# Kernel optimization log

Measured on AMD Instinct MI355X. Metric: run time of the kernel, lower is better.

## Reference

```python
import jax, jax.numpy as jnp
import numpy as np

LAMBDA_1 = 1.0
LAMBDA_2 = 0.5


def setup_inputs() -> dict:
    key = jax.random.key(0)
    k1, k2, k3, k4, k5 = jax.random.split(key, 5)
    N_TRAIN, N_UNL, C = 4096, 32768, 1000
    G, K = 512, 64
    return {
        "train_logits": jax.random.normal(k1, (N_TRAIN, C), dtype=jnp.float32),
        "train_targets": jax.random.randint(k2, (N_TRAIN,), 0, C, dtype=jnp.int64),
        "unlabeled_logits": jax.random.normal(k3, (N_UNL, C), dtype=jnp.float32),
        "centroid_ids": jax.random.randint(k4, (G,), 0, N_TRAIN, dtype=jnp.int64),
        "member_ids": jax.random.randint(k5, (G, K), 0, N_UNL, dtype=jnp.int64),
    }


def reference(train_logits, train_targets, unlabeled_logits, centroid_ids, member_ids):
    N_unl = unlabeled_logits.shape[0]
    G, K = member_ids.shape

    # --- cross-entropy (mean) ---
    logp = jax.nn.log_softmax(train_logits, axis=-1)
    ce = -jnp.mean(jnp.take_along_axis(logp, train_targets[:, None], axis=1))

    # --- gather group tensors ---
    centroids = train_logits[centroid_ids]          # [G, C]
    members = unlabeled_logits[member_ids]          # [G, K, C]

    # --- alignment: sum_g sum_k ||centroid_g - member_gk||_2 / N_unl ---
    align = jnp.sum(jnp.linalg.norm(centroids[:, None, :] - members, axis=-1)) / N_unl

    # --- robustness: per-group upper-triangle pairwise L2 sums / (K * N_unl) ---
    sq = jnp.sum(members * members, axis=-1)                       # [G, K]
    gram = jnp.einsum("gkc,glc->gkl", members, members)            # [G, K, K]
    d2 = jnp.maximum(sq[:, :, None] + sq[:, None, :] - 2.0 * gram, 0.0)
    dist = jnp.sqrt(jnp.where(d2 > 0, d2, 1.0)) * (d2 > 0)         # safe sqrt
    iu = jnp.triu(jnp.ones((K, K), dtype=dist.dtype), k=1)         # i < j pairs
    robust = jnp.sum(dist * iu) / (K * N_unl)

    return ce + LAMBDA_1 * align + LAMBDA_2 * robust
```

## Files before the change

kernel.cpp:

```cpp
#include <hip/hip_runtime.h>
#include <hip/hip_bf16.h>

#define N_TRAIN 4096
#define N_UNL   32768
#define C_DIM   1000
#define G_GRP   512
#define K_MEM   64
#define CPAD    1024

typedef short          short8 __attribute__((ext_vector_type(8)));
typedef float          f32x4  __attribute__((ext_vector_type(4)));
typedef unsigned short us4    __attribute__((ext_vector_type(4)));

__device__ __forceinline__ unsigned short f2bf(float f) {
    unsigned int u = __float_as_uint(f);
    u += 0x7fffu + ((u >> 16) & 1u);
    return (unsigned short)(u >> 16);
}

__device__ __forceinline__ void async16(void* ldsdst, const void* gsrc) {
    __builtin_amdgcn_global_load_lds(
        (const __attribute__((address_space(1))) unsigned int*)gsrc,
        (__attribute__((address_space(3))) unsigned int*)ldsdst,
        16, 0, 0);
}

__global__ __launch_bounds__(256) void conv_kernel(const float* __restrict__ unl,
                                                   const float* __restrict__ train,
                                                   const int*   __restrict__ cids,
                                                   unsigned short* __restrict__ bf_unl,
                                                   unsigned short* __restrict__ bf_cent) {
    const int total = (N_UNL + G_GRP) * 256;
    for (int s = blockIdx.x * 256 + threadIdx.x; s < total; s += gridDim.x * 256) {
        const int row = s >> 8;
        const int t   = s & 255;
        const float* src;
        unsigned short* dst;
        if (row < N_UNL) {
            src = unl + (long)row * C_DIM;
            dst = bf_unl + (long)row * CPAD;
        } else {
            const int g = row - N_UNL;
            src = train + (long)cids[g] * C_DIM;
            dst = bf_cent + (long)g * CPAD;
        }
        us4 h = (us4){0, 0, 0, 0};
        if (t < 250) {
            float4 v = *(const float4*)(src + t * 4);
            h[0] = f2bf(v.x); h[1] = f2bf(v.y); h[2] = f2bf(v.z); h[3] = f2bf(v.w);
        }
        *(us4*)(dst + t * 4) = h;
    }
}

__global__ __launch_bounds__(256) void ce_kernel(const float* __restrict__ logits,
                                                 const int*   __restrict__ targets,
                                                 float* __restrict__ part) {
    const int wave = threadIdx.x >> 6;
    const int lane = threadIdx.x & 63;
    const int row  = blockIdx.x * 4 + wave;
    const float* rp = logits + (long)row * C_DIM;
    __shared__ float pr[4];

    float x[16];
#pragma unroll
    for (int i = 0; i < 16; ++i) {
        int c = lane + i * 64;
        x[i] = (c < C_DIM) ? rp[c] : -1e30f;
    }
    float m = x[0];
#pragma unroll
    for (int i = 1; i < 16; ++i) m = fmaxf(m, x[i]);
#pragma unroll
    for (int off = 32; off > 0; off >>= 1) m = fmaxf(m, __shfl_xor(m, off, 64));

    float s = 0.f;
#pragma unroll
    for (int i = 0; i < 16; ++i) s += __expf(x[i] - m);
#pragma unroll
    for (int off = 32; off > 0; off >>= 1) s += __shfl_xor(s, off, 64);

    if (lane == 0) {
        int t = targets[row];
        pr[wave] = -(rp[t] - m - __logf(s));
    }
    __syncthreads();
    if (threadIdx.x == 0)
        part[blockIdx.x] = (pr[0] + pr[1] + pr[2] + pr[3]) * (1.0f / (float)N_TRAIN);
}

#define PAIR_PITCH 1040
#define NPAIRS     40
#define LDSZ       (NPAIRS * PAIR_PITCH)

__global__ __launch_bounds__(256) void group_kernel(const unsigned short* __restrict__ bf_unl,
                                                    const unsigned short* __restrict__ bf_cent,
                                                    const int* __restrict__ member_ids,
                                                    float* __restrict__ part) {
    __shared__ __align__(16) unsigned char lds[LDSZ];
    __shared__ float sq_sh[K_MEM];
    __shared__ float red_sh[256];
    __shared__ float sqc_sh;

    const int g    = blockIdx.x;
    const int tid  = threadIdx.x;
    const int w    = tid >> 6;
    const int lane = tid & 63;
    const int quad = lane >> 4;
    const int c16  = lane & 15;

    const int mid = member_ids[g * K_MEM + lane];

    {
        const int base = 32 * PAIR_PITCH + 512;
        for (int off = tid * 16; off < LDSZ - base; off += 256 * 16)
            *(float4*)(lds + base + off) = make_float4(0.f, 0.f, 0.f, 0.f);
    }

    f32x4 acc[4], accC, accD;
#pragma unroll
    for (int t = 0; t < 4; ++t) acc[t] = (f32x4){0.f, 0.f, 0.f, 0.f};
    accC = (f32x4){0.f, 0.f, 0.f, 0.f};
    accD = (f32x4){0.f, 0.f, 0.f, 0.f};

    const unsigned offB0 = (unsigned)(c16 >> 1) * PAIR_PITCH + (unsigned)(c16 & 1) * 512;
    const unsigned offA  = offB0 + (unsigned)w * (8 * PAIR_PITCH);
    const unsigned offC  = offB0 + 32u * PAIR_PITCH;

    for (int ch = 0; ch < 4; ++ch) {
        const int colB = ch * 256;
#pragma unroll
        for (int i = 0; i < 8; ++i) {
            const int p = w * 8 + i;
            const int r = 2 * p + (lane >> 5);
            const int rid = __shfl(mid, r, 64);
            const unsigned short* src = bf_unl + (long)rid * CPAD + colB + (lane & 31) * 8;
            async16(lds + p * PAIR_PITCH, src);
        }
        if (w == 1 && lane < 32) {
            const unsigned short* src = bf_cent + (long)g * CPAD + colB + (lane & 31) * 8;
            async16(lds + 32 * PAIR_PITCH, src);
        }
        __syncthreads();

#pragma unroll
        for (int s = 0; s < 8; ++s) {
            const unsigned kb = (unsigned)(s * 32 + quad * 8) * 2;
            short8 b0 = *(const short8*)(lds + offB0 + 0 * 8 * PAIR_PITCH + kb);
            short8 b1 = *(const short8*)(lds + offB0 + 1 * 8 * PAIR_PITCH + kb);
            short8 b2 = *(const short8*)(lds + offB0 + 2 * 8 * PAIR_PITCH + kb);
            short8 b3 = *(const short8*)(lds + offB0 + 3 * 8 * PAIR_PITCH + kb);
            short8 aM = *(const short8*)(lds + offA + kb);
            short8 aC = *(const short8*)(lds + offC + kb);
            acc[0] = __builtin_amdgcn_mfma_f32_16x16x32_bf16(aM, b0, acc[0], 0, 0, 0);
            acc[1] = __builtin_amdgcn_mfma_f32_16x16x32_bf16(aM, b1, acc[1], 0, 0, 0);
            acc[2] = __builtin_amdgcn_mfma_f32_16x16x32_bf16(aM, b2, acc[2], 0, 0, 0);
            acc[3] = __builtin_amdgcn_mfma_f32_16x16x32_bf16(aM, b3, acc[3], 0, 0, 0);
            accC   = __builtin_amdgcn_mfma_f32_16x16x32_bf16(aC, aM, accC, 0, 0, 0);
            if (w == 0)
                accD = __builtin_amdgcn_mfma_f32_16x16x32_bf16(aC, aC, accD, 0, 0, 0);
        }
        __syncthreads();
    }

#pragma unroll
    for (int t = 0; t < 4; ++t) {
        if (t == w) {
#pragma unroll
            for (int r = 0; r < 4; ++r)
                if (c16 == quad * 4 + r) sq_sh[w * 16 + c16] = acc[t][r];
        }
    }
    if (tid == 0) sqc_sh = accD[0];
    __syncthreads();

    float local = 0.f;
    if (quad == 0) {
        const int j = w * 16 + c16;
        const float d2 = sqc_sh + sq_sh[j] - 2.f * accC[0];
        if (d2 > 0.f) local += sqrtf(d2) * (1.0f / (float)N_UNL);
    }
#pragma unroll
    for (int t = 0; t < 4; ++t) {
#pragma unroll
        for (int r = 0; r < 4; ++r) {
            const int i = w * 16 + quad * 4 + r;
            const int j = t * 16 + c16;
            if (j > i) {
                const float d2 = sq_sh[i] + sq_sh[j] - 2.f * acc[t][r];
                if (d2 > 0.f)
                    local += sqrtf(d2) * (0.5f / ((float)K_MEM * (float)N_UNL));
            }
        }
    }

    red_sh[tid] = local;
    __syncthreads();
#pragma unroll
    for (int s = 128; s > 0; s >>= 1) {
        if (tid < s) red_sh[tid] += red_sh[tid + s];
        __syncthreads();
    }
    if (tid == 0) part[N_TRAIN / 4 + g] = red_sh[0];
}

__global__ __launch_bounds__(256) void final_kernel(const float* __restrict__ part,
                                                    float* __restrict__ out, int out_size) {
    __shared__ float red[256];
    float s = 0.f;
    for (int i = threadIdx.x; i < N_TRAIN / 4 + G_GRP; i += 256) s += part[i];
    red[threadIdx.x] = s;
    __syncthreads();
#pragma unroll
    for (int st = 128; st > 0; st >>= 1) {
        if (threadIdx.x < st) red[threadIdx.x] += red[threadIdx.x + st];
        __syncthreads();
    }
    if (threadIdx.x == 0) out[0] = red[0];
    for (int i = 1 + threadIdx.x; i < out_size; i += 256) out[i] = 0.f;
}

extern "C" void kernel_launch(void* const* d_in, const int* in_sizes, int n_in,
                              void* d_out, int out_size, void* d_ws, size_t ws_size,
                              hipStream_t stream) {
    (void)in_sizes; (void)n_in; (void)ws_size;
    const float* train_logits  = (const float*)d_in[0];
    const int*   train_targets = (const int*)d_in[1];
    const float* unl           = (const float*)d_in[2];
    const int*   centroid_ids  = (const int*)d_in[3];
    const int*   member_ids    = (const int*)d_in[4];
    float* out = (float*)d_out;

    char* ws = (char*)d_ws;
    unsigned short* bf_unl  = (unsigned short*)ws;
    unsigned short* bf_cent = (unsigned short*)(ws + (size_t)N_UNL * CPAD * 2);
    float* part = (float*)(ws + (size_t)(N_UNL + G_GRP) * CPAD * 2);

    conv_kernel<<<4096, 256, 0, stream>>>(unl, train_logits, centroid_ids, bf_unl, bf_cent);
    ce_kernel<<<N_TRAIN / 4, 256, 0, stream>>>(train_logits, train_targets, part);
    group_kernel<<<G_GRP, 256, 0, stream>>>(bf_unl, bf_cent, member_ids, part);
    final_kernel<<<1, 256, 0, stream>>>(part, out, out_size);
}
```

Baseline: 240.9 us.

## Fuse bf16 conversion into group kernel and merge CE into one launch

Removes the separate pass that converts every unlabeled row to bf16. Each group block now gathers its fp32 member rows directly, converts them in registers and stores the bf16 values to LDS. CE blocks are appended to the same grid, which removes two launches and lets CE overlap the group work. This avoids writing and re-reading a full bf16 copy of the unlabeled matrix. The trade-off is synchronous global loads in place of async LDS loads, and a simpler rounding in pack_bf.

Measured after the change: 217.1 us. 1.11x faster.

```diff
diff --git a/kernel.cpp b/kernel.cpp
--- a/kernel.cpp
+++ b/kernel.cpp
@@ -1,121 +1,97 @@
 #include <hip/hip_runtime.h>
-#include <hip/hip_bf16.h>
 
 #define N_TRAIN 4096
 #define N_UNL   32768
 #define C_DIM   1000
 #define G_GRP   512
 #define K_MEM   64
-#define CPAD    1024
-
-typedef short          short8 __attribute__((ext_vector_type(8)));
-typedef float          f32x4  __attribute__((ext_vector_type(4)));
-typedef unsigned short us4    __attribute__((ext_vector_type(4)));
-
-__device__ __forceinline__ unsigned short f2bf(float f) {
-    unsigned int u = __float_as_uint(f);
-    u += 0x7fffu + ((u >> 16) & 1u);
-    return (unsigned short)(u >> 16);
-}
-
-__device__ __forceinline__ void async16(void* ldsdst, const void* gsrc) {
-    __builtin_amdgcn_global_load_lds(
-        (const __attribute__((address_space(1))) unsigned int*)gsrc,
-        (__attribute__((address_space(3))) unsigned int*)ldsdst,
-        16, 0, 0);
-}
-
-__global__ __launch_bounds__(256) void conv_kernel(const float* __restrict__ unl,
-                                                   const float* __restrict__ train,
-                                                   const int*   __restrict__ cids,
-                                                   unsigned short* __restrict__ bf_unl,
-                                                   unsigned short* __restrict__ bf_cent) {
-    const int total = (N_UNL + G_GRP) * 256;
-    for (int s = blockIdx.x * 256 + threadIdx.x; s < total; s += gridDim.x * 256) {
-        const int row = s >> 8;
-        const int t   = s & 255;
-        const float* src;
-        unsigned short* dst;
-        if (row < N_UNL) {
-            src = unl + (long)row * C_DIM;
-            dst = bf_unl + (long)row * CPAD;
-        } else {
-            const int g = row - N_UNL;
-            src = train + (long)cids[g] * C_DIM;
-            dst = bf_cent + (long)g * CPAD;
-        }
-        us4 h = (us4){0, 0, 0, 0};
-        if (t < 250) {
-            float4 v = *(const float4*)(src + t * 4);
-            h[0] = f2bf(v.x); h[1] = f2bf(v.y); h[2] = f2bf(v.z); h[3] = f2bf(v.w);
-        }
-        *(us4*)(dst + t * 4) = h;
-    }
-}
-
-__global__ __launch_bounds__(256) void ce_kernel(const float* __restrict__ logits,
-                                                 const int*   __restrict__ targets,
-                                                 float* __restrict__ part) {
-    const int wave = threadIdx.x >> 6;
-    const int lane = threadIdx.x & 63;
-    const int row  = blockIdx.x * 4 + wave;
-    const float* rp = logits + (long)row * C_DIM;
-    __shared__ float pr[4];
-
-    float x[16];
-#pragma unroll
-    for (int i = 0; i < 16; ++i) {
-        int c = lane + i * 64;
-        x[i] = (c < C_DIM) ? rp[c] : -1e30f;
-    }
-    float m = x[0];
-#pragma unroll
-    for (int i = 1; i < 16; ++i) m = fmaxf(m, x[i]);
-#pragma unroll
-    for (int off = 32; off > 0; off >>= 1) m = fmaxf(m, __shfl_xor(m, off, 64));
-
-    float s = 0.f;
-#pragma unroll
-    for (int i = 0; i < 16; ++i) s += __expf(x[i] - m);
-#pragma unroll
-    for (int off = 32; off > 0; off >>= 1) s += __shfl_xor(s, off, 64);
-
-    if (lane == 0) {
-        int t = targets[row];
-        pr[wave] = -(rp[t] - m - __logf(s));
-    }
-    __syncthreads();
-    if (threadIdx.x == 0)
-        part[blockIdx.x] = (pr[0] + pr[1] + pr[2] + pr[3]) * (1.0f / (float)N_TRAIN);
-}
-
-#define PAIR_PITCH 1040
-#define NPAIRS     40
-#define LDSZ       (NPAIRS * PAIR_PITCH)
-
-__global__ __launch_bounds__(256) void group_kernel(const unsigned short* __restrict__ bf_unl,
-                                                    const unsigned short* __restrict__ bf_cent,
-                                                    const int* __restrict__ member_ids,
+
+#define CE_BLOCKS (N_TRAIN / 16)
+#define NPART     (G_GRP + CE_BLOCKS)
+
+#define PITCH_B 528
+#define ROWS    80
+
+typedef short        short8 __attribute__((ext_vector_type(8)));
+typedef float        f32x4  __attribute__((ext_vector_type(4)));
+typedef unsigned int u32x4  __attribute__((ext_vector_type(4)));
+
+__device__ __forceinline__ unsigned int pack_bf(float a, float b) {
+    unsigned int ua = __float_as_uint(a) + 0x8000u;
+    unsigned int ub = __float_as_uint(b) + 0x8000u;
+    return (ua >> 16) | (ub & 0xffff0000u);
+}
+
+__global__ __launch_bounds__(256) void fused_kernel(const float* __restrict__ train,
+                                                    const int*   __restrict__ targets,
+                                                    const float* __restrict__ unl,
+                                                    const int*   __restrict__ cids,
+                                                    const int*   __restrict__ mids,
                                                     float* __restrict__ part) {
-    __shared__ __align__(16) unsigned char lds[LDSZ];
+    __shared__ __align__(16) unsigned short bf[ROWS * (PITCH_B / 2)];
+    __shared__ int   ids_sh[K_MEM];
     __shared__ float sq_sh[K_MEM];
     __shared__ float red_sh[256];
     __shared__ float sqc_sh;
 
-    const int g    = blockIdx.x;
     const int tid  = threadIdx.x;
     const int w    = tid >> 6;
     const int lane = tid & 63;
+
+    if (blockIdx.x >= G_GRP) {
+        const int blk = (int)blockIdx.x - G_GRP;
+        float ce = 0.f;
+        for (int r4 = 0; r4 < 4; ++r4) {
+            const int row = blk * 16 + w * 4 + r4;
+            const float* rp = train + (long)row * C_DIM;
+            float x[16];
+#pragma unroll
+            for (int i = 0; i < 16; ++i) {
+                int c = lane + i * 64;
+                x[i] = (c < C_DIM) ? rp[c] : -1e30f;
+            }
+            float m = x[0];
+#pragma unroll
+            for (int i = 1; i < 16; ++i) m = fmaxf(m, x[i]);
+#pragma unroll
+            for (int off = 32; off > 0; off >>= 1) m = fmaxf(m, __shfl_xor(m, off, 64));
+            float s = 0.f;
+#pragma unroll
+            for (int i = 0; i < 16; ++i) s += __expf(x[i] - m);
+#pragma unroll
+            for (int off = 32; off > 0; off >>= 1) s += __shfl_xor(s, off, 64);
+            if (lane == 0) {
+                int t = targets[row];
+                ce += -(rp[t] - m - __logf(s));
+            }
+        }
+        if (lane == 0) red_sh[w] = ce;
+        __syncthreads();
+        if (tid == 0)
+            part[G_GRP + blk] = (red_sh[0] + red_sh[1] + red_sh[2] + red_sh[3]) *
+                                (1.0f / (float)N_TRAIN);
+        return;
+    }
+
+    const int g    = blockIdx.x;
     const int quad = lane >> 4;
     const int c16  = lane & 15;
 
-    const int mid = member_ids[g * K_MEM + lane];
-
-    {
-        const int base = 32 * PAIR_PITCH + 512;
-        for (int off = tid * 16; off < LDSZ - base; off += 256 * 16)
-            *(float4*)(lds + base + off) = make_float4(0.f, 0.f, 0.f, 0.f);
-    }
+    for (int idx = tid; idx < 495; idx += 256)
+        *(u32x4*)((char*)bf + 65 * PITCH_B + idx * 16) = (u32x4){0, 0, 0, 0};
+    if (tid < K_MEM) ids_sh[tid] = mids[g * K_MEM + tid];
+    __syncthreads();
+
+    const int rgrp = tid >> 5;
+    const int l32  = tid & 31;
+    const int colf = l32 * 8;
+    const int cid  = cids[g];
+
+    const float* srcb[8];
+#pragma unroll
+    for (int i = 0; i < 8; ++i)
+        srcb[i] = unl + (long)ids_sh[rgrp + 8 * i] * C_DIM + colf;
+    const float* csrc = train + (long)cid * C_DIM + colf;
 
     f32x4 acc[4], accC, accD;
 #pragma unroll
@@ -123,35 +99,39 @@
     accC = (f32x4){0.f, 0.f, 0.f, 0.f};
     accD = (f32x4){0.f, 0.f, 0.f, 0.f};
 
-    const unsigned offB0 = (unsigned)(c16 >> 1) * PAIR_PITCH + (unsigned)(c16 & 1) * 512;
-    const unsigned offA  = offB0 + (unsigned)w * (8 * PAIR_PITCH);
-    const unsigned offC  = offB0 + 32u * PAIR_PITCH;
+    const float4 z4 = make_float4(0.f, 0.f, 0.f, 0.f);
 
     for (int ch = 0; ch < 4; ++ch) {
-        const int colB = ch * 256;
+        const int col = ch * 256 + colf;
+        const bool v0 = (col < C_DIM);
+        const bool v1 = (col + 4 < C_DIM);
 #pragma unroll
         for (int i = 0; i < 8; ++i) {
-            const int p = w * 8 + i;
-            const int r = 2 * p + (lane >> 5);
-            const int rid = __shfl(mid, r, 64);
-            const unsigned short* src = bf_unl + (long)rid * CPAD + colB + (lane & 31) * 8;
-            async16(lds + p * PAIR_PITCH, src);
-        }
-        if (w == 1 && lane < 32) {
-            const unsigned short* src = bf_cent + (long)g * CPAD + colB + (lane & 31) * 8;
-            async16(lds + 32 * PAIR_PITCH, src);
+            float4 a = v0 ? *(const float4*)(srcb[i] + ch * 256) : z4;
+            float4 b = v1 ? *(const float4*)(srcb[i] + ch * 256 + 4) : z4;
+            u32x4 h = {pack_bf(a.x, a.y), pack_bf(a.z, a.w),
+                       pack_bf(b.x, b.y), pack_bf(b.z, b.w)};
+            *(u32x4*)((char*)bf + (rgrp + 8 * i) * PITCH_B + colf * 2) = h;
+        }
+        if (tid < 32) {
+            float4 a = v0 ? *(const float4*)(csrc + ch * 256) : z4;
+            float4 b = v1 ? *(const float4*)(csrc + ch * 256 + 4) : z4;
+            u32x4 h = {pack_bf(a.x, a.y), pack_bf(a.z, a.w),
+                       pack_bf(b.x, b.y), pack_bf(b.z, b.w)};
+            *(u32x4*)((char*)bf + 64 * PITCH_B + colf * 2) = h;
         }
         __syncthreads();
 
 #pragma unroll
         for (int s = 0; s < 8; ++s) {
-            const unsigned kb = (unsigned)(s * 32 + quad * 8) * 2;
-            short8 b0 = *(const short8*)(lds + offB0 + 0 * 8 * PAIR_PITCH + kb);
-            short8 b1 = *(const short8*)(lds + offB0 + 1 * 8 * PAIR_PITCH + kb);
-            short8 b2 = *(const short8*)(lds + offB0 + 2 * 8 * PAIR_PITCH + kb);
-            short8 b3 = *(const short8*)(lds + offB0 + 3 * 8 * PAIR_PITCH + kb);
-            short8 aM = *(const short8*)(lds + offA + kb);
-            short8 aC = *(const short8*)(lds + offC + kb);
+            const int kbb = s * 64 + quad * 16;
+            const char* base = (const char*)bf;
+            short8 b0 = *(const short8*)(base + (0 * 16 + c16) * PITCH_B + kbb);
+            short8 b1 = *(const short8*)(base + (1 * 16 + c16) * PITCH_B + kbb);
+            short8 b2 = *(const short8*)(base + (2 * 16 + c16) * PITCH_B + kbb);
+            short8 b3 = *(const short8*)(base + (3 * 16 + c16) * PITCH_B + kbb);
+            short8 aM = *(const short8*)(base + (w * 16 + c16) * PITCH_B + kbb);
+            short8 aC = *(const short8*)(base + (64 + c16) * PITCH_B + kbb);
             acc[0] = __builtin_amdgcn_mfma_f32_16x16x32_bf16(aM, b0, acc[0], 0, 0, 0);
             acc[1] = __builtin_amdgcn_mfma_f32_16x16x32_bf16(aM, b1, acc[1], 0, 0, 0);
             acc[2] = __builtin_amdgcn_mfma_f32_16x16x32_bf16(aM, b2, acc[2], 0, 0, 0);
@@ -201,14 +181,14 @@
         if (tid < s) red_sh[tid] += red_sh[tid + s];
         __syncthreads();
     }
-    if (tid == 0) part[N_TRAIN / 4 + g] = red_sh[0];
+    if (tid == 0) part[g] = red_sh[0];
 }
 
 __global__ __launch_bounds__(256) void final_kernel(const float* __restrict__ part,
                                                     float* __restrict__ out, int out_size) {
     __shared__ float red[256];
     float s = 0.f;
-    for (int i = threadIdx.x; i < N_TRAIN / 4 + G_GRP; i += 256) s += part[i];
+    for (int i = threadIdx.x; i < NPART; i += 256) s += part[i];
     red[threadIdx.x] = s;
     __syncthreads();
 #pragma unroll
@@ -229,15 +209,10 @@
     const float* unl           = (const float*)d_in[2];
     const int*   centroid_ids  = (const int*)d_in[3];
     const int*   member_ids    = (const int*)d_in[4];
-    float* out = (float*)d_out;
-
-    char* ws = (char*)d_ws;
-    unsigned short* bf_unl  = (unsigned short*)ws;
-    unsigned short* bf_cent = (unsigned short*)(ws + (size_t)N_UNL * CPAD * 2);
-    float* part = (float*)(ws + (size_t)(N_UNL + G_GRP) * CPAD * 2);
-
-    conv_kernel<<<4096, 256, 0, stream>>>(unl, train_logits, centroid_ids, bf_unl, bf_cent);
-    ce_kernel<<<N_TRAIN / 4, 256, 0, stream>>>(train_logits, train_targets, part);
-    group_kernel<<<G_GRP, 256, 0, stream>>>(bf_unl, bf_cent, member_ids, part);
+    float* out  = (float*)d_out;
+    float* part = (float*)d_ws;
+
+    fused_kernel<<<NPART, 256, 0, stream>>>(train_logits, train_targets, unl,
+                                            centroid_ids, member_ids, part);
     final_kernel<<<1, 256, 0, stream>>>(part, out, out_size);
 }
```
